# Kernel tuning notes

Measured on AMD Instinct MI355X. Metric: run time of the kernel, lower is better.

## Reference

```python
import jax, jax.numpy as jnp
import numpy as np

N, L, D = 64, 510, 768
L1, K, OUT = 128, 20, 300
EPS = 1e-5


def _make_spans(key, n, n_spans, max_len):
    ks, kl = jax.random.split(key)
    starts = jnp.sort(jax.random.randint(ks, (n, n_spans), 0, max_len - 4), axis=1)
    lens = jax.random.randint(kl, (n, n_spans), 1, 5)
    ends = jnp.minimum(starts + lens, max_len)
    return starts.astype(jnp.int32), ends.astype(jnp.int32)


def setup_inputs() -> dict:
    key = jax.random.key(0)
    ks = jax.random.split(key, 10)
    t1 = jax.random.normal(ks[0], (N, L, D), jnp.float32)
    encoded_know = jax.random.normal(ks[1], (N, L, D), jnp.float32)
    span_starts, span_ends = _make_spans(ks[2], N, L1, L)
    know_span_starts, know_span_ends = _make_spans(ks[3], N, K, L)
    # padding masks: True = masked; guarantee >=1 valid entry per row
    valid1 = jax.random.randint(ks[4], (N,), L1 // 2, L1 + 1)
    key_padding_mask = jnp.arange(L1)[None, :] >= valid1[:, None]
    validk = jax.random.randint(ks[5], (N,), 5, K + 1)
    key_padding_mask_know = jnp.arange(K)[None, :] >= validk[:, None]
    W_lin = jax.random.normal(ks[6], (OUT, D), jnp.float32) * 0.02
    b_lin = jnp.zeros((OUT,), jnp.float32)
    gamma = jnp.ones((OUT,), jnp.float32)
    beta = jnp.zeros((OUT,), jnp.float32)
    W_score = jax.random.normal(ks[7], (1, OUT), jnp.float32) * 0.02
    b_score = jnp.zeros((1,), jnp.float32)
    return dict(t1=t1, encoded_know=encoded_know,
                span_starts=span_starts, span_ends=span_ends,
                key_padding_mask=key_padding_mask,
                know_span_starts=know_span_starts, know_span_ends=know_span_ends,
                key_padding_mask_know=key_padding_mask_know,
                W_lin=W_lin, b_lin=b_lin, gamma=gamma, beta=beta,
                W_score=W_score, b_score=b_score)


def _span_mean(x, starts, ends):
    # x: (N,L,D); spans [s,e) -> mean via inclusive-scan difference (one pass)
    n, l, d = x.shape
    cs = jnp.concatenate([jnp.zeros((n, 1, d), x.dtype), jnp.cumsum(x, axis=1)], axis=1)
    gather = lambda idx: jnp.take_along_axis(cs, idx[:, :, None].astype(jnp.int32), axis=1)
    sums = gather(ends) - gather(starts)  # (N, n_spans, D)
    lens = jnp.maximum(ends - starts, 1).astype(x.dtype)[:, :, None]
    return sums / lens


def _layernorm(x, g, b):
    m = jnp.mean(x, axis=-1, keepdims=True)
    v = jnp.mean(jnp.square(x - m), axis=-1, keepdims=True)
    return (x - m) * jax.lax.rsqrt(v + EPS) * g + b


def reference(t1, encoded_know, span_starts, span_ends, key_padding_mask,
              know_span_starts, know_span_ends, key_padding_mask_know,
              W_lin, b_lin, gamma, beta, W_score, b_score):
    lam = 1.0

    def branch(x, s, e, mask):
        pooled = _span_mean(x, s, e)                       # ragged segment mean
        h = _layernorm(pooled @ W_lin.T + b_lin, gamma, beta)
        sc = (h @ W_score.T + b_score)[..., 0]             # (N, n_spans)
        sc = jnp.where(mask, -jnp.inf, sc)                 # masked_fill
        return h, jax.nn.softmax(sc * lam, axis=1)

    h1, s1 = branch(t1, span_starts, span_ends, key_padding_mask)
    hk, sk = branch(encoded_know, know_span_starts, know_span_ends, key_padding_mask_know)
    score = jnp.broadcast_to(s1[:, :, None], h1.shape)     # repeat to (N,L1,OUT)
    return h1, score, hk, sk
```

## Files before the change

### kernel.cpp

```cpp
#include <hip/hip_runtime.h>
#include <hip/hip_bf16.h>
#include <stdint.h>

#define NB    64
#define LSEQ  510
#define DIN   768
#define L1S   128
#define KS    20
#define OUTF  300
#define NPAD  320
#define EPSL  1e-5f

#define M1    (NB * L1S)
#define MK    (NB * KS)
#define MT    (M1 + MK)

#define OFF_H1    0
#define OFF_SCORE (M1 * OUTF)
#define OFF_HK    (2 * M1 * OUTF)
#define OFF_SK    (OFF_HK + MK * OUTF)

#define WS_FLAG    0
#define WS_SCORES  64
#define WS_WBF     81920
#define WS_POOLED  1048576
#define WS_NEEDED  (WS_POOLED + (size_t)MT * DIN * 2)

typedef short  short8_t  __attribute__((ext_vector_type(8)));
typedef float  float4v_t __attribute__((ext_vector_type(4)));
typedef unsigned short ushort4_t __attribute__((ext_vector_type(4)));
typedef unsigned short ushort8_t __attribute__((ext_vector_type(8)));

#define SA_STRIDE 776
#define SC_STRIDE 324
#define LDS_BYTES 41984

__device__ inline bool mask_at(const void* m, int idx, int flag) {
    switch (flag) {
        case 1:  return ((const unsigned char*)m)[idx] != 0;
        case 2:  return ((const float*)m)[idx] != 0.0f;
        case 3:  return ((const unsigned short*)m)[idx] != 0;
        default: return ((const int*)m)[idx] != 0;
    }
}

__global__ __launch_bounds__(256)
void prep_kernel(const unsigned int* __restrict__ p, int* __restrict__ flag,
                 const float* __restrict__ W, unsigned short* __restrict__ Wb) {
    if (blockIdx.x == 0) {
        __shared__ int f_bf16, f_f32, f_other;
        if (threadIdx.x == 0) { f_bf16 = 0; f_f32 = 0; f_other = 0; }
        __syncthreads();
        for (int i = threadIdx.x; i < 2048; i += blockDim.x) {
            unsigned int v = p[i];
            if (v <= 1u) continue;
            if (v == 0x3F803F80u)       atomicOr(&f_bf16, 1);
            else if (v == 0x3F800000u)  atomicOr(&f_f32, 1);
            else                        atomicOr(&f_other, 1);
        }
        __syncthreads();
        if (threadIdx.x == 0) {
            int f = 0;
            if (f_bf16)       f = 3;
            else if (f_f32)   f = 2;
            else if (f_other) f = 1;
            *flag = f;
        }
        return;
    }
    int idx = (blockIdx.x - 1) * 256 + threadIdx.x;
    if (idx >= NPAD * DIN) return;
    int r = idx / DIN;
    float v = (r < OUTF) ? W[idx] : 0.f;
    __hip_bfloat16 b = __float2bfloat16(v);
    Wb[idx] = *(unsigned short*)&b;
}

__global__ __launch_bounds__(256)
void pool_kernel(const float* __restrict__ t1, const float* __restrict__ know,
                 const int* __restrict__ s1s, const int* __restrict__ s1e,
                 const int* __restrict__ kss, const int* __restrict__ kse,
                 unsigned short* __restrict__ pooled) {
    const int idx = blockIdx.x * 256 + threadIdx.x;
    const int g  = idx / 192;
    const int c4 = idx - g * 192;
    int s, e;
    const float* src;
    if (g < M1) {
        s = s1s[g]; e = s1e[g];
        src = t1 + (size_t)(g >> 7) * (LSEQ * DIN);
    } else {
        int gg = g - M1;
        s = kss[gg]; e = kse[gg];
        src = know + (size_t)(gg / KS) * (LSEQ * DIN);
    }
    if (s < 0) s = 0;
    if (e > LSEQ) e = LSEQ;
    int len = e - s; if (len < 1) len = 1;

    const float4* p = (const float4*)src + s * 192 + c4;
    const float4 z = {0.f, 0.f, 0.f, 0.f};
    float4 v0 = p[0];
    float4 v1 = z, v2 = z, v3 = z;
    if (len > 1) v1 = p[1 * 192];
    if (len > 2) v2 = p[2 * 192];
    if (len > 3) v3 = p[3 * 192];
    float4 acc;
    acc.x = (v0.x + v1.x) + (v2.x + v3.x);
    acc.y = (v0.y + v1.y) + (v2.y + v3.y);
    acc.z = (v0.z + v1.z) + (v2.z + v3.z);
    acc.w = (v0.w + v1.w) + (v2.w + v3.w);
    for (int r = 4; r < len; ++r) {
        float4 v = p[r * 192];
        acc.x += v.x; acc.y += v.y; acc.z += v.z; acc.w += v.w;
    }
    const float inv = 1.0f / (float)len;
    __hip_bfloat16 b0 = __float2bfloat16(acc.x * inv);
    __hip_bfloat16 b1 = __float2bfloat16(acc.y * inv);
    __hip_bfloat16 b2 = __float2bfloat16(acc.z * inv);
    __hip_bfloat16 b3 = __float2bfloat16(acc.w * inv);
    ushort4_t pk;
    pk.x = *(unsigned short*)&b0; pk.y = *(unsigned short*)&b1;
    pk.z = *(unsigned short*)&b2; pk.w = *(unsigned short*)&b3;
    *(ushort4_t*)(pooled + (size_t)g * DIN + c4 * 4) = pk;
}

__global__ __launch_bounds__(640, 5)
void gemm_kernel(const unsigned short* __restrict__ pooled,
                 const unsigned short* __restrict__ Wb,
                 const float* __restrict__ bias,
                 const float* __restrict__ gamma,
                 const float* __restrict__ beta,
                 const float* __restrict__ Wsc,
                 const float* __restrict__ bsc,
                 float* __restrict__ out,
                 float* __restrict__ scores) {
    __shared__ unsigned long long lds_raw[LDS_BYTES / 8];
    unsigned short* sA = (unsigned short*)lds_raw;

    const int tid = threadIdx.x;
    const int R0  = blockIdx.x * 16;
    const bool isk = (R0 >= M1);

    for (int t = tid; t < 16 * 96; t += 640) {
        int sp = t / 96;
        int c8 = t - sp * 96;
        ushort8_t v = *(const ushort8_t*)(pooled + (size_t)(R0 + sp) * DIN + c8 * 8);
        *(ushort8_t*)(sA + sp * SA_STRIDE + c8 * 8) = v;
    }
    __syncthreads();

    const int wave = tid >> 6;
    const int lane = tid & 63;
    const int quad = lane >> 4;
    const int l16  = lane & 15;
    const int cg   = wave % 5;
    const int kh   = wave / 5;

    const unsigned short* sArow = sA + l16 * SA_STRIDE + quad * 8 + kh * 384;
    const unsigned short* bb = Wb + (size_t)(cg * 64 + l16) * DIN + quad * 8 + kh * 384;

    float4v_t acc0 = {0.f, 0.f, 0.f, 0.f};
    float4v_t acc1 = {0.f, 0.f, 0.f, 0.f};
    float4v_t acc2 = {0.f, 0.f, 0.f, 0.f};
    float4v_t acc3 = {0.f, 0.f, 0.f, 0.f};

#pragma unroll 4
    for (int k0 = 0; k0 < 384; k0 += 32) {
        short8_t a  = *(const short8_t*)(sArow + k0);
        short8_t b0 = *(const short8_t*)(bb + 0 * 16 * DIN + k0);
        short8_t b1 = *(const short8_t*)(bb + 1 * 16 * DIN + k0);
        short8_t b2 = *(const short8_t*)(bb + 2 * 16 * DIN + k0);
        short8_t b3 = *(const short8_t*)(bb + 3 * 16 * DIN + k0);
        acc0 = __builtin_amdgcn_mfma_f32_16x16x32_bf16(a, b0, acc0, 0, 0, 0);
        acc1 = __builtin_amdgcn_mfma_f32_16x16x32_bf16(a, b1, acc1, 0, 0, 0);
        acc2 = __builtin_amdgcn_mfma_f32_16x16x32_bf16(a, b2, acc2, 0, 0, 0);
        acc3 = __builtin_amdgcn_mfma_f32_16x16x32_bf16(a, b3, acc3, 0, 0, 0);
    }

    __syncthreads();
    float* sC = (float*)lds_raw;
#pragma unroll
    for (int i = 0; i < 4; ++i) {
        int r = (kh * 16 + quad * 4 + i) * SC_STRIDE + cg * 64 + l16;
        sC[r +  0] = acc0[i];
        sC[r + 16] = acc1[i];
        sC[r + 32] = acc2[i];
        sC[r + 48] = acc3[i];
    }
    __syncthreads();

    if (wave < 8) {
        const float bs0 = bsc[0];
#pragma unroll
        for (int rr = 0; rr < 2; ++rr) {
            const int r = wave * 2 + rr;
            const int g = R0 + r;
            float tv[5];
            float s = 0.f;
#pragma unroll
            for (int m = 0; m < 5; ++m) {
                int c = lane + 64 * m;
                float v = 0.f;
                if (c < OUTF)
                    v = sC[r * SC_STRIDE + c] + sC[(16 + r) * SC_STRIDE + c] + bias[c];
                tv[m] = v; s += v;
            }
#pragma unroll
            for (int off = 32; off > 0; off >>= 1) s += __shfl_xor(s, off, 64);
            const float mean = s * (1.0f / OUTF);
            float vs = 0.f;
#pragma unroll
            for (int m = 0; m < 5; ++m) {
                int c = lane + 64 * m;
                float d = (c < OUTF) ? (tv[m] - mean) : 0.f;
                vs += d * d;
            }
#pragma unroll
            for (int off = 32; off > 0; off >>= 1) vs += __shfl_xor(vs, off, 64);
            const float rstd = rsqrtf(vs * (1.0f / OUTF) + EPSL);

            const size_t off0 = isk ? (size_t)OFF_HK + (size_t)(g - M1) * OUTF
                                    : (size_t)g * OUTF;
            float sc = 0.f;
#pragma unroll
            for (int m = 0; m < 5; ++m) {
                int c = lane + 64 * m;
                if (c < OUTF) {
                    float h = (tv[m] - mean) * rstd * gamma[c] + beta[c];
                    out[off0 + c] = h;
                    sc += h * Wsc[c];
                }
            }
#pragma unroll
            for (int off = 32; off > 0; off >>= 1) sc += __shfl_xor(sc, off, 64);
            if (lane == 0) scores[g] = sc + bs0;
        }
    }
}

__global__ __launch_bounds__(640, 5)
void fused_gemm_kernel(const float* __restrict__ t1,
                       const float* __restrict__ know,
                       const int* __restrict__ s1s, const int* __restrict__ s1e,
                       const int* __restrict__ kss, const int* __restrict__ kse,
                       const unsigned short* __restrict__ Wb,
                       const float* __restrict__ bias,
                       const float* __restrict__ gamma,
                       const float* __restrict__ beta,
                       const float* __restrict__ Wsc,
                       const float* __restrict__ bsc,
                       float* __restrict__ out,
                       float* __restrict__ scores) {
    __shared__ unsigned long long lds_raw[LDS_BYTES / 8];
    unsigned short* sA   = (unsigned short*)lds_raw;
    int*   sSrc = (int*)  ((char*)lds_raw + 16 * 1552);
    int*   sLen = (int*)  ((char*)lds_raw + 16 * 1552 + 64);
    float* sInv = (float*)((char*)lds_raw + 16 * 1552 + 128);

    const int tid = threadIdx.x;
    const int R0  = blockIdx.x * 16;
    const bool isk = (R0 >= M1);

    if (tid < 16) {
        int g = R0 + tid;
        int s, e, n;
        if (!isk) { n = g >> 7;          s = s1s[g];      e = s1e[g]; }
        else      { int gg = g - M1; n = gg / KS; s = kss[gg]; e = kse[gg]; }
        if (s < 0) s = 0;
        if (e > LSEQ) e = LSEQ;
        int len = e - s; if (len < 1) len = 1;
        sSrc[tid] = n * (LSEQ * (DIN / 4)) + s * (DIN / 4);
        sLen[tid] = len;
        sInv[tid] = 1.0f / (float)len;
    }
    __syncthreads();

    const float4* src4 = (const float4*)(isk ? know : t1);
    for (int t = tid; t < 16 * 192; t += 640) {
        int sp = t / 192;
        int c4 = t - sp * 192;
        const float4* p = src4 + sSrc[sp] + c4;
        int len = sLen[sp];
        const float4 z = {0.f, 0.f, 0.f, 0.f};
        float4 v0 = p[0];
        float4 v1 = z, v2 = z, v3 = z;
        if (len > 1) v1 = p[1 * 192];
        if (len > 2) v2 = p[2 * 192];
        if (len > 3) v3 = p[3 * 192];
        float4 acc;
        acc.x = (v0.x + v1.x) + (v2.x + v3.x);
        acc.y = (v0.y + v1.y) + (v2.y + v3.y);
        acc.z = (v0.z + v1.z) + (v2.z + v3.z);
        acc.w = (v0.w + v1.w) + (v2.w + v3.w);
        for (int r = 4; r < len; ++r) {
            float4 v = p[r * 192];
            acc.x += v.x; acc.y += v.y; acc.z += v.z; acc.w += v.w;
        }
        float inv = sInv[sp];
        __hip_bfloat16 b0 = __float2bfloat16(acc.x * inv);
        __hip_bfloat16 b1 = __float2bfloat16(acc.y * inv);
        __hip_bfloat16 b2 = __float2bfloat16(acc.z * inv);
        __hip_bfloat16 b3 = __float2bfloat16(acc.w * inv);
        ushort4_t pk;
        pk.x = *(unsigned short*)&b0; pk.y = *(unsigned short*)&b1;
        pk.z = *(unsigned short*)&b2; pk.w = *(unsigned short*)&b3;
        *(ushort4_t*)(sA + sp * SA_STRIDE + c4 * 4) = pk;
    }
    __syncthreads();

    const int wave = tid >> 6;
    const int lane = tid & 63;
    const int quad = lane >> 4;
    const int l16  = lane & 15;
    const int cg   = wave % 5;
    const int kh   = wave / 5;

    const unsigned short* sArow = sA + l16 * SA_STRIDE + quad * 8 + kh * 384;
    const unsigned short* bb = Wb + (size_t)(cg * 64 + l16) * DIN + quad * 8 + kh * 384;

    float4v_t acc0 = {0.f, 0.f, 0.f, 0.f};
    float4v_t acc1 = {0.f, 0.f, 0.f, 0.f};
    float4v_t acc2 = {0.f, 0.f, 0.f, 0.f};
    float4v_t acc3 = {0.f, 0.f, 0.f, 0.f};

#pragma unroll 4
    for (int k0 = 0; k0 < 384; k0 += 32) {
        short8_t a  = *(const short8_t*)(sArow + k0);
        short8_t b0 = *(const short8_t*)(bb + 0 * 16 * DIN + k0);
        short8_t b1 = *(const short8_t*)(bb + 1 * 16 * DIN + k0);
        short8_t b2 = *(const short8_t*)(bb + 2 * 16 * DIN + k0);
        short8_t b3 = *(const short8_t*)(bb + 3 * 16 * DIN + k0);
        acc0 = __builtin_amdgcn_mfma_f32_16x16x32_bf16(a, b0, acc0, 0, 0, 0);
        acc1 = __builtin_amdgcn_mfma_f32_16x16x32_bf16(a, b1, acc1, 0, 0, 0);
        acc2 = __builtin_amdgcn_mfma_f32_16x16x32_bf16(a, b2, acc2, 0, 0, 0);
        acc3 = __builtin_amdgcn_mfma_f32_16x16x32_bf16(a, b3, acc3, 0, 0, 0);
    }

    __syncthreads();
    float* sC = (float*)lds_raw;
#pragma unroll
    for (int i = 0; i < 4; ++i) {
        int r = (kh * 16 + quad * 4 + i) * SC_STRIDE + cg * 64 + l16;
        sC[r +  0] = acc0[i];
        sC[r + 16] = acc1[i];
        sC[r + 32] = acc2[i];
        sC[r + 48] = acc3[i];
    }
    __syncthreads();

    if (wave < 8) {
        const float bs0 = bsc[0];
#pragma unroll
        for (int rr = 0; rr < 2; ++rr) {
            const int r = wave * 2 + rr;
            const int g = R0 + r;
            float tv[5];
            float s = 0.f;
#pragma unroll
            for (int m = 0; m < 5; ++m) {
                int c = lane + 64 * m;
                float v = 0.f;
                if (c < OUTF)
                    v = sC[r * SC_STRIDE + c] + sC[(16 + r) * SC_STRIDE + c] + bias[c];
                tv[m] = v; s += v;
            }
#pragma unroll
            for (int off = 32; off > 0; off >>= 1) s += __shfl_xor(s, off, 64);
            const float mean = s * (1.0f / OUTF);
            float vs = 0.f;
#pragma unroll
            for (int m = 0; m < 5; ++m) {
                int c = lane + 64 * m;
                float d = (c < OUTF) ? (tv[m] - mean) : 0.f;
                vs += d * d;
            }
#pragma unroll
            for (int off = 32; off > 0; off >>= 1) vs += __shfl_xor(vs, off, 64);
            const float rstd = rsqrtf(vs * (1.0f / OUTF) + EPSL);

            const size_t off0 = isk ? (size_t)OFF_HK + (size_t)(g - M1) * OUTF
                                    : (size_t)g * OUTF;
            float sc = 0.f;
#pragma unroll
            for (int m = 0; m < 5; ++m) {
                int c = lane + 64 * m;
                if (c < OUTF) {
                    float h = (tv[m] - mean) * rstd * gamma[c] + beta[c];
                    out[off0 + c] = h;
                    sc += h * Wsc[c];
                }
            }
#pragma unroll
            for (int off = 32; off > 0; off >>= 1) sc += __shfl_xor(sc, off, 64);
            if (lane == 0) scores[g] = sc + bs0;
        }
    }
}

__global__ __launch_bounds__(128)
void softmax_bcast_kernel(const float* __restrict__ scores,
                          const void* __restrict__ m1,
                          const void* __restrict__ mk,
                          const int* __restrict__ flagp,
                          float* __restrict__ out) {
    const int flag = *flagp;
    const int b = blockIdx.x;
    const int tid = threadIdx.x;
    const int lane = tid & 63;

    if (b < NB * 5) {
        __shared__ float sprob[L1S];
        const int n = b / 5;
        const int chunk = b - n * 5;
        if (tid < 64) {
            float v0 = scores[n * L1S + lane];
            float v1 = scores[n * L1S + lane + 64];
            if (mask_at(m1, n * L1S + lane, flag))      v0 = -INFINITY;
            if (mask_at(m1, n * L1S + lane + 64, flag)) v1 = -INFINITY;
            float mx = fmaxf(v0, v1);
#pragma unroll
            for (int off = 32; off > 0; off >>= 1) mx = fmaxf(mx, __shfl_xor(mx, off, 64));
            float e0 = __expf(v0 - mx);
            float e1 = __expf(v1 - mx);
            float s = e0 + e1;
#pragma unroll
            for (int off = 32; off > 0; off >>= 1) s += __shfl_xor(s, off, 64);
            float inv = 1.0f / s;
            sprob[lane]      = e0 * inv;
            sprob[lane + 64] = e1 * inv;
        }
        __syncthreads();
        float* dst = out + (size_t)OFF_SCORE + (size_t)n * (L1S * OUTF);
        const int cbase = chunk * 7680;
#pragma unroll
        for (int i = 0; i < 15; ++i) {
            int e0i = cbase + (i * 128 + tid) * 4;
            float4 v;
            v.x = sprob[(e0i + 0) / OUTF];
            v.y = sprob[(e0i + 1) / OUTF];
            v.z = sprob[(e0i + 2) / OUTF];
            v.w = sprob[(e0i + 3) / OUTF];
            *(float4*)(dst + e0i) = v;
        }
    } else {
        const int n = (b - NB * 5) * 2 + (tid >> 6);
        float v = -INFINITY;
        if (lane < KS) {
            v = scores[M1 + n * KS + lane];
            if (mask_at(mk, n * KS + lane, flag)) v = -INFINITY;
        }
        float mx = v;
#pragma unroll
        for (int off = 32; off > 0; off >>= 1) mx = fmaxf(mx, __shfl_xor(mx, off, 64));
        float e = (lane < KS) ? __expf(v - mx) : 0.f;
        float s = e;
#pragma unroll
        for (int off = 32; off > 0; off >>= 1) s += __shfl_xor(s, off, 64);
        if (lane < KS) out[(size_t)OFF_SK + n * KS + lane] = e / s;
    }
}

extern "C" void kernel_launch(void* const* d_in, const int* in_sizes, int n_in,
                              void* d_out, int out_size, void* d_ws, size_t ws_size,
                              hipStream_t stream) {
    const float* t1   = (const float*)d_in[0];
    const float* know = (const float*)d_in[1];
    const int* s1s = (const int*)d_in[2];
    const int* s1e = (const int*)d_in[3];
    const void* m1 = d_in[4];
    const int* kss = (const int*)d_in[5];
    const int* kse = (const int*)d_in[6];
    const void* mk = d_in[7];
    const float* Wl  = (const float*)d_in[8];
    const float* bl  = (const float*)d_in[9];
    const float* gm  = (const float*)d_in[10];
    const float* bt  = (const float*)d_in[11];
    const float* Wsc = (const float*)d_in[12];
    const float* bsc = (const float*)d_in[13];
    float* out = (float*)d_out;

    char* ws = (char*)d_ws;
    int*            flag   = (int*)(ws + WS_FLAG);
    float*          scores = (float*)(ws + WS_SCORES);
    unsigned short* Wb     = (unsigned short*)(ws + WS_WBF);
    unsigned short* pooled = (unsigned short*)(ws + WS_POOLED);

    prep_kernel<<<1 + (NPAD * DIN + 255) / 256, 256, 0, stream>>>(
        (const unsigned int*)m1, flag, Wl, Wb);

    if (ws_size >= WS_NEEDED) {
        pool_kernel<<<(MT * 192) / 256, 256, 0, stream>>>(t1, know, s1s, s1e,
                                                          kss, kse, pooled);
        gemm_kernel<<<MT / 16, 640, 0, stream>>>(pooled, Wb, bl, gm, bt,
                                                 Wsc, bsc, out, scores);
    } else {
        fused_gemm_kernel<<<MT / 16, 640, 0, stream>>>(t1, know, s1s, s1e,
                                                       kss, kse, Wb, bl, gm,
                                                       bt, Wsc, bsc, out, scores);
    }
    softmax_bcast_kernel<<<NB * 5 + NB / 2, 128, 0, stream>>>(scores, m1, mk,
                                                              flag, out);
}
```

Measured before the change: 268.6 us.

## Split GEMM+LayerNorm into fine-grained GEMM kernel and separate LN kernel

Replaces the 640-thread GEMM kernel, which staged pooled rows in LDS and fused LayerNorm and scoring, with two kernels. The first is a single-wave MFMA GEMM that handles a 16x32 tile over the full K and writes fp32 pre-activations to a workspace buffer. The second applies bias, LayerNorm and the score dot product, one wave per row. This trades the LDS staging and the K-split reduction for many more small blocks, aiming at higher parallelism. The cost is an extra global round-trip of the hpre buffer, one more launch, and a larger workspace requirement, which may push execution onto the fused fallback path.

```diff
diff --git a/kernel.cpp b/kernel.cpp
--- a/kernel.cpp
+++ b/kernel.cpp
@@ -24,7 +24,8 @@
 #define WS_SCORES  64
 #define WS_WBF     81920
 #define WS_POOLED  1048576
-#define WS_NEEDED  (WS_POOLED + (size_t)MT * DIN * 2)
+#define WS_HPRE    16777216
+#define WS_NEEDED  (WS_HPRE + (size_t)MT * NPAD * 4)
 
 typedef short  short8_t  __attribute__((ext_vector_type(8)));
 typedef float  float4v_t __attribute__((ext_vector_type(4)));
@@ -125,118 +126,95 @@
     *(ushort4_t*)(pooled + (size_t)g * DIN + c4 * 4) = pk;
 }
 
-__global__ __launch_bounds__(640, 5)
-void gemm_kernel(const unsigned short* __restrict__ pooled,
-                 const unsigned short* __restrict__ Wb,
-                 const float* __restrict__ bias,
-                 const float* __restrict__ gamma,
-                 const float* __restrict__ beta,
-                 const float* __restrict__ Wsc,
-                 const float* __restrict__ bsc,
-                 float* __restrict__ out,
-                 float* __restrict__ scores) {
-    __shared__ unsigned long long lds_raw[LDS_BYTES / 8];
-    unsigned short* sA = (unsigned short*)lds_raw;
-
-    const int tid = threadIdx.x;
-    const int R0  = blockIdx.x * 16;
-    const bool isk = (R0 >= M1);
-
-    for (int t = tid; t < 16 * 96; t += 640) {
-        int sp = t / 96;
-        int c8 = t - sp * 96;
-        ushort8_t v = *(const ushort8_t*)(pooled + (size_t)(R0 + sp) * DIN + c8 * 8);
-        *(ushort8_t*)(sA + sp * SA_STRIDE + c8 * 8) = v;
-    }
-    __syncthreads();
-
-    const int wave = tid >> 6;
-    const int lane = tid & 63;
+__global__ __launch_bounds__(64)
+void gemm3_kernel(const unsigned short* __restrict__ pooled,
+                  const unsigned short* __restrict__ Wb,
+                  float* __restrict__ hpre) {
+    const int b   = blockIdx.x;
+    const int rb  = b / 10;
+    const int cgb = b - rb * 10;
+    const int R0  = rb * 16;
+    const int lane = threadIdx.x;
     const int quad = lane >> 4;
     const int l16  = lane & 15;
-    const int cg   = wave % 5;
-    const int kh   = wave / 5;
-
-    const unsigned short* sArow = sA + l16 * SA_STRIDE + quad * 8 + kh * 384;
-    const unsigned short* bb = Wb + (size_t)(cg * 64 + l16) * DIN + quad * 8 + kh * 384;
+
+    const unsigned short* arow = pooled + (size_t)(R0 + l16) * DIN + quad * 8;
+    const unsigned short* bb0  = Wb + (size_t)(cgb * 32 + l16) * DIN + quad * 8;
+    const unsigned short* bb1  = bb0 + 16 * DIN;
 
     float4v_t acc0 = {0.f, 0.f, 0.f, 0.f};
     float4v_t acc1 = {0.f, 0.f, 0.f, 0.f};
-    float4v_t acc2 = {0.f, 0.f, 0.f, 0.f};
-    float4v_t acc3 = {0.f, 0.f, 0.f, 0.f};
 
 #pragma unroll 4
-    for (int k0 = 0; k0 < 384; k0 += 32) {
-        short8_t a  = *(const short8_t*)(sArow + k0);
-        short8_t b0 = *(const short8_t*)(bb + 0 * 16 * DIN + k0);
-        short8_t b1 = *(const short8_t*)(bb + 1 * 16 * DIN + k0);
-        short8_t b2 = *(const short8_t*)(bb + 2 * 16 * DIN + k0);
-        short8_t b3 = *(const short8_t*)(bb + 3 * 16 * DIN + k0);
+    for (int k0 = 0; k0 < DIN; k0 += 32) {
+        short8_t a  = *(const short8_t*)(arow + k0);
+        short8_t b0 = *(const short8_t*)(bb0 + k0);
+        short8_t b1 = *(const short8_t*)(bb1 + k0);
         acc0 = __builtin_amdgcn_mfma_f32_16x16x32_bf16(a, b0, acc0, 0, 0, 0);
         acc1 = __builtin_amdgcn_mfma_f32_16x16x32_bf16(a, b1, acc1, 0, 0, 0);
-        acc2 = __builtin_amdgcn_mfma_f32_16x16x32_bf16(a, b2, acc2, 0, 0, 0);
-        acc3 = __builtin_amdgcn_mfma_f32_16x16x32_bf16(a, b3, acc3, 0, 0, 0);
-    }
-
-    __syncthreads();
-    float* sC = (float*)lds_raw;
+    }
+
 #pragma unroll
     for (int i = 0; i < 4; ++i) {
-        int r = (kh * 16 + quad * 4 + i) * SC_STRIDE + cg * 64 + l16;
-        sC[r +  0] = acc0[i];
-        sC[r + 16] = acc1[i];
-        sC[r + 32] = acc2[i];
-        sC[r + 48] = acc3[i];
-    }
-    __syncthreads();
-
-    if (wave < 8) {
-        const float bs0 = bsc[0];
-#pragma unroll
-        for (int rr = 0; rr < 2; ++rr) {
-            const int r = wave * 2 + rr;
-            const int g = R0 + r;
-            float tv[5];
-            float s = 0.f;
-#pragma unroll
-            for (int m = 0; m < 5; ++m) {
-                int c = lane + 64 * m;
-                float v = 0.f;
-                if (c < OUTF)
-                    v = sC[r * SC_STRIDE + c] + sC[(16 + r) * SC_STRIDE + c] + bias[c];
-                tv[m] = v; s += v;
-            }
-#pragma unroll
-            for (int off = 32; off > 0; off >>= 1) s += __shfl_xor(s, off, 64);
-            const float mean = s * (1.0f / OUTF);
-            float vs = 0.f;
-#pragma unroll
-            for (int m = 0; m < 5; ++m) {
-                int c = lane + 64 * m;
-                float d = (c < OUTF) ? (tv[m] - mean) : 0.f;
-                vs += d * d;
-            }
-#pragma unroll
-            for (int off = 32; off > 0; off >>= 1) vs += __shfl_xor(vs, off, 64);
-            const float rstd = rsqrtf(vs * (1.0f / OUTF) + EPSL);
-
-            const size_t off0 = isk ? (size_t)OFF_HK + (size_t)(g - M1) * OUTF
-                                    : (size_t)g * OUTF;
-            float sc = 0.f;
-#pragma unroll
-            for (int m = 0; m < 5; ++m) {
-                int c = lane + 64 * m;
-                if (c < OUTF) {
-                    float h = (tv[m] - mean) * rstd * gamma[c] + beta[c];
-                    out[off0 + c] = h;
-                    sc += h * Wsc[c];
-                }
-            }
-#pragma unroll
-            for (int off = 32; off > 0; off >>= 1) sc += __shfl_xor(sc, off, 64);
-            if (lane == 0) scores[g] = sc + bs0;
-        }
-    }
+        const size_t r = (size_t)(R0 + quad * 4 + i) * NPAD + cgb * 32 + l16;
+        hpre[r]      = acc0[i];
+        hpre[r + 16] = acc1[i];
+    }
+}
+
+__global__ __launch_bounds__(512)
+void ln_kernel(const float* __restrict__ hpre,
+               const float* __restrict__ bias,
+               const float* __restrict__ gamma,
+               const float* __restrict__ beta,
+               const float* __restrict__ Wsc,
+               const float* __restrict__ bsc,
+               float* __restrict__ out,
+               float* __restrict__ scores) {
+    const int wave = threadIdx.x >> 6;
+    const int lane = threadIdx.x & 63;
+    const int g = blockIdx.x * 8 + wave;
+    const float bs0 = bsc[0];
+
+    float tv[5];
+    float s = 0.f;
+#pragma unroll
+    for (int m = 0; m < 5; ++m) {
+        int c = lane + 64 * m;
+        float v = 0.f;
+        if (c < OUTF)
+            v = hpre[(size_t)g * NPAD + c] + bias[c];
+        tv[m] = v; s += v;
+    }
+#pragma unroll
+    for (int off = 32; off > 0; off >>= 1) s += __shfl_xor(s, off, 64);
+    const float mean = s * (1.0f / OUTF);
+    float vs = 0.f;
+#pragma unroll
+    for (int m = 0; m < 5; ++m) {
+        int c = lane + 64 * m;
+        float d = (c < OUTF) ? (tv[m] - mean) : 0.f;
+        vs += d * d;
+    }
+#pragma unroll
+    for (int off = 32; off > 0; off >>= 1) vs += __shfl_xor(vs, off, 64);
+    const float rstd = rsqrtf(vs * (1.0f / OUTF) + EPSL);
+
+    const size_t off0 = (g < M1) ? (size_t)g * OUTF
+                                 : (size_t)OFF_HK + (size_t)(g - M1) * OUTF;
+    float sc = 0.f;
+#pragma unroll
+    for (int m = 0; m < 5; ++m) {
+        int c = lane + 64 * m;
+        if (c < OUTF) {
+            float h = (tv[m] - mean) * rstd * gamma[c] + beta[c];
+            out[off0 + c] = h;
+            sc += h * Wsc[c];
+        }
+    }
+#pragma unroll
+    for (int off = 32; off > 0; off >>= 1) sc += __shfl_xor(sc, off, 64);
+    if (lane == 0) scores[g] = sc + bs0;
 }
 
 __global__ __launch_bounds__(640, 5)
@@ -485,6 +463,7 @@
     float*          scores = (float*)(ws + WS_SCORES);
     unsigned short* Wb     = (unsigned short*)(ws + WS_WBF);
     unsigned short* pooled = (unsigned short*)(ws + WS_POOLED);
+    float*          hpre   = (float*)(ws + WS_HPRE);
 
     prep_kernel<<<1 + (NPAD * DIN + 255) / 256, 256, 0, stream>>>(
         (const unsigned int*)m1, flag, Wl, Wb);
@@ -492,8 +471,9 @@
     if (ws_size >= WS_NEEDED) {
         pool_kernel<<<(MT * 192) / 256, 256, 0, stream>>>(t1, know, s1s, s1e,
                                                           kss, kse, pooled);
-        gemm_kernel<<<MT / 16, 640, 0, stream>>>(pooled, Wb, bl, gm, bt,
-                                                 Wsc, bsc, out, scores);
+        gemm3_kernel<<<(MT / 16) * (NPAD / 32), 64, 0, stream>>>(pooled, Wb, hpre);
+        ln_kernel<<<MT / 8, 512, 0, stream>>>(hpre, bl, gm, bt, Wsc, bsc,
+                                              out, scores);
     } else {
         fused_gemm_kernel<<<MT / 16, 640, 0, stream>>>(t1, know, s1s, s1e,
                                                        kss, kse, Wb, bl, gm,
```

Result: slower. 276.1 us (+2.8%).
